# Kernel optimization log

Hardware: AMD Instinct MI355X
Metric: run time of the kernel (lower is better)

Reference implementation:

```python
import jax, jax.numpy as jnp
import numpy as np


def _derive_cayley():
    basis_gens = [(), (1,), (2,), (3,), (1, 2), (1, 3), (2, 3), (1, 2, 3)]
    gens_to_idx = {g: i for i, g in enumerate(basis_gens)}

    def reduce(a, b):
        gens = list(a) + list(b)
        sign = 1
        changed = True
        while changed:
            changed = False
            i = 0
            while i < len(gens) - 1:
                if gens[i] == gens[i + 1]:
                    gens.pop(i); gens.pop(i)
                    changed = True
                    if i > 0:
                        i -= 1
                elif gens[i] > gens[i + 1]:
                    gens[i], gens[i + 1] = gens[i + 1], gens[i]
                    sign *= -1
                    changed = True
                    i += 1
                else:
                    i += 1
        return gens_to_idx[tuple(gens)], sign

    K = np.zeros((8, 8), dtype=np.int32)   # target blade of product i*j
    S = np.zeros((8, 8), dtype=np.float32)  # sign of product i*j
    for i in range(8):
        for j in range(8):
            k, s = reduce(basis_gens[i], basis_gens[j])
            K[i, j] = k
            S[i, j] = s
    return K, S

_K, _S = _derive_cayley()
_I, _J = np.meshgrid(np.arange(8), np.arange(8), indexing='ij')
_K_FLAT = jnp.asarray(_K.reshape(-1))
_I_FLAT = jnp.asarray(_I.reshape(-1))
_J_FLAT = jnp.asarray(_J.reshape(-1))
_S_FLAT = jnp.asarray(_S.reshape(-1))

LN_EPS = 1e-5


def setup_inputs() -> dict:
    key = jax.random.key(0)
    ks = jax.random.split(key, 4)
    N_tok, D, F = 4096, 1024, 4096
    x = jax.random.normal(ks[0], (N_tok, 8, D), dtype=jnp.float32)
    interaction_weights = jnp.ones((64,), dtype=jnp.float32) * 0.1
    geo_gate = jnp.asarray(0.5, dtype=jnp.float32)
    ln_w = jnp.ones((D,), dtype=jnp.float32)
    ln_b = jnp.zeros((D,), dtype=jnp.float32)
    s = 0.02
    w_gate = jax.random.normal(ks[1], (D, F), dtype=jnp.float32) * s
    w_up = jax.random.normal(ks[2], (D, F), dtype=jnp.float32) * s
    w_down = jax.random.normal(ks[3], (F, D), dtype=jnp.float32) * s
    return {"x": x, "interaction_weights": interaction_weights, "geo_gate": geo_gate,
            "ln_w": ln_w, "ln_b": ln_b, "w_gate": w_gate, "w_up": w_up, "w_down": w_down}


def reference(x, interaction_weights, geo_gate, ln_w, ln_b, w_gate, w_up, w_down):
    dtype = x.dtype
    # sparse bilinear coefficient tensor C[k, i, j] = sign(i,j) * sigmoid(w)[i*8+j]
    w = jax.nn.sigmoid(interaction_weights).astype(dtype)  # (64,)
    C = jnp.zeros((8, 8, 8), dtype=dtype).at[_K_FLAT, _I_FLAT, _J_FLAT].set(_S_FLAT.astype(dtype) * w)
    # geometric product: geo[n,k,d] = sum_ij C[k,i,j] x[n,i,d] x[n,j,d]
    geo = jnp.einsum('kij,nid,njd->nkd', C, x, x)
    g = jax.nn.sigmoid(geo_gate).astype(dtype)
    mixed = g * geo + (1.0 - g) * x  # (N, 8, D)
    # LayerNorm over last dim D
    mu = jnp.mean(mixed, axis=-1, keepdims=True)
    var = jnp.mean(jnp.square(mixed - mu), axis=-1, keepdims=True)
    flat = (mixed - mu) * jax.lax.rsqrt(var + LN_EPS) * ln_w + ln_b
    # SwiGLU MLP
    h = jax.nn.silu(flat @ w_gate) * (flat @ w_up)  # (N, 8, F)
    out = h @ w_down  # (N, 8, D)
    return x + out
```

## Files before the change

kernel.cpp:

```cpp
#include <hip/hip_runtime.h>

typedef unsigned short u16;
using bf16x8 = __attribute__((ext_vector_type(8))) __bf16;
using f32x4  = __attribute__((ext_vector_type(4))) float;
using u16x4  = __attribute__((ext_vector_type(4))) unsigned short;

#define D_DIM 1024
#define F_DIM 4096

struct Cayley { int k[8][8]; int s[8][8]; };
constexpr Cayley make_cayley() {
    Cayley c{};
    const int gens[8][3] = {{0,0,0},{1,0,0},{2,0,0},{3,0,0},{1,2,0},{1,3,0},{2,3,0},{1,2,3}};
    const int glen[8] = {0,1,1,1,2,2,2,3};
    const int mask2idx[8] = {0,1,2,4,3,5,6,7};
    for (int i = 0; i < 8; ++i) {
        for (int j = 0; j < 8; ++j) {
            int g[6] = {0,0,0,0,0,0};
            int n = 0;
            for (int t = 0; t < glen[i]; ++t) g[n++] = gens[i][t];
            for (int t = 0; t < glen[j]; ++t) g[n++] = gens[j][t];
            int sign = 1;
            bool changed = true;
            while (changed) {
                changed = false;
                int t = 0;
                while (t + 1 < n) {
                    if (g[t] == g[t+1]) {
                        for (int u = t; u + 2 < n; ++u) g[u] = g[u+2];
                        n -= 2; changed = true;
                        if (t > 0) --t;
                    } else if (g[t] > g[t+1]) {
                        int tmp = g[t]; g[t] = g[t+1]; g[t+1] = tmp;
                        sign = -sign; changed = true; ++t;
                    } else {
                        ++t;
                    }
                }
            }
            int mask = 0;
            for (int t = 0; t < n; ++t) mask |= 1 << (g[t] - 1);
            c.k[i][j] = mask2idx[mask];
            c.s[i][j] = sign;
        }
    }
    return c;
}
constexpr Cayley CAY = make_cayley();

__device__ __forceinline__ u16 f2bf(float f) {
    unsigned u = __float_as_uint(f);
    unsigned r = 0x7FFFu + ((u >> 16) & 1u);
    return (u16)((u + r) >> 16);
}

__device__ __forceinline__ void gload16(const u16* g, const u16* l) {
    __builtin_amdgcn_global_load_lds(
        (const __attribute__((address_space(1))) void*)g,
        (__attribute__((address_space(3))) void*)l, 16, 0, 0);
}

__device__ __forceinline__ bf16x8 frag(const u16* tile, int row, int ks, int lane) {
    const int slot = ((ks << 2) + (lane >> 4)) ^ (lane & 7);
    return *(const bf16x8*)(tile + row * 64 + slot * 8);
}

__global__ __launch_bounds__(256) void transpose_kernel(
    const float* __restrict__ in, u16* __restrict__ outp, int R, int C, int mode)
{
    __shared__ float tile[32][33];
    const int tx = threadIdx.x & 31, ty = threadIdx.x >> 5;
    const int c0 = blockIdx.x * 32, r0 = blockIdx.y * 32;
    #pragma unroll
    for (int t = 0; t < 4; ++t)
        tile[ty + t*8][tx] = in[(size_t)(r0 + ty + t*8) * C + c0 + tx];
    __syncthreads();
    #pragma unroll
    for (int t = 0; t < 4; ++t) {
        const int c = c0 + ty + t*8;
        int orow;
        if (mode == 0)      orow = c;
        else if (mode == 1) orow = ((c >> 4) << 5) + (c & 15);
        else                orow = ((c >> 4) << 5) + 16 + (c & 15);
        outp[(size_t)orow * R + r0 + tx] = f2bf(tile[tx][ty + t*8]);
    }
}

__global__ __launch_bounds__(256, 2) void geo_ln_kernel(
    const float* __restrict__ x, const float* __restrict__ iw,
    const float* __restrict__ gg, const float* __restrict__ lnw,
    const float* __restrict__ lnb, u16* __restrict__ flat)
{
    __shared__ float wsig[64];
    __shared__ float red[4][16];
    const int tid = threadIdx.x;
    if (tid < 64) wsig[tid] = 1.f / (1.f + __expf(-iw[tid]));
    __syncthreads();
    const float g   = 1.f / (1.f + __expf(-gg[0]));
    const float gm1 = 1.f - g;

    float coef[64];
    #pragma unroll
    for (int t = 0; t < 64; ++t) coef[t] = (float)CAY.s[t >> 3][t & 7] * wsig[t];

    const int n  = blockIdx.x;
    const int d0 = tid * 4;
    const float* xb = x + (size_t)n * 8 * D_DIM;
    f32x4 xv[8];
    #pragma unroll
    for (int i = 0; i < 8; ++i) xv[i] = __builtin_nontemporal_load((const f32x4*)(xb + i * D_DIM + d0));

    float mix[8][4];
    #pragma unroll
    for (int s4 = 0; s4 < 4; ++s4) {
        float xs[8];
        #pragma unroll
        for (int i = 0; i < 8; ++i) xs[i] = xv[i][s4];
        float geo[8] = {0.f,0.f,0.f,0.f,0.f,0.f,0.f,0.f};
        #pragma unroll
        for (int i = 0; i < 8; ++i) {
            #pragma unroll
            for (int j = 0; j < 8; ++j) {
                geo[CAY.k[i][j]] = fmaf(coef[i*8+j] * xs[i], xs[j], geo[CAY.k[i][j]]);
            }
        }
        #pragma unroll
        for (int k = 0; k < 8; ++k) mix[k][s4] = g * geo[k] + gm1 * xs[k];
    }

    float s1[8], s2[8];
    #pragma unroll
    for (int k = 0; k < 8; ++k) {
        s1[k] = 0.f; s2[k] = 0.f;
        #pragma unroll
        for (int s4 = 0; s4 < 4; ++s4) {
            s1[k] += mix[k][s4];
            s2[k]  = fmaf(mix[k][s4], mix[k][s4], s2[k]);
        }
    }
    #pragma unroll
    for (int m = 1; m < 64; m <<= 1) {
        #pragma unroll
        for (int k = 0; k < 8; ++k) {
            s1[k] += __shfl_xor(s1[k], m, 64);
            s2[k] += __shfl_xor(s2[k], m, 64);
        }
    }
    const int wave = tid >> 6, lane = tid & 63;
    if (lane == 0) {
        #pragma unroll
        for (int k = 0; k < 8; ++k) { red[wave][k] = s1[k]; red[wave][8+k] = s2[k]; }
    }
    __syncthreads();
    float mean[8], rstd[8];
    #pragma unroll
    for (int k = 0; k < 8; ++k) {
        float a = red[0][k] + red[1][k] + red[2][k] + red[3][k];
        float b = red[0][8+k] + red[1][8+k] + red[2][8+k] + red[3][8+k];
        float mu  = a * (1.f / 1024.f);
        float var = b * (1.f / 1024.f) - mu * mu;
        mean[k] = mu;
        rstd[k] = rsqrtf(var + 1e-5f);
    }
    f32x4 lw = *(const f32x4*)(lnw + d0);
    f32x4 lb = *(const f32x4*)(lnb + d0);
    #pragma unroll
    for (int k = 0; k < 8; ++k) {
        u16x4 o;
        #pragma unroll
        for (int s4 = 0; s4 < 4; ++s4) {
            float v = (mix[k][s4] - mean[k]) * rstd[k] * lw[s4] + lb[s4];
            o[s4] = f2bf(v);
        }
        *(u16x4*)(flat + ((size_t)(n * 8 + k)) * D_DIM + d0) = o;
    }
}

template<int KDIM, bool S1, bool S2, int W1, int W4>
__device__ __forceinline__ void ktile(
    int t, const u16* __restrict__ A, const u16* __restrict__ B,
    u16 (*As)[256][64], u16 (*Bs)[256][64],
    int brow, int bcol, int wave, int lane, int wm, int wn, int fr,
    f32x4 (&acc)[8][4])
{
    const int buf = t & 1;
    const u16* At = &As[buf][0][0];
    const u16* Bt = &Bs[buf][0][0];
    const int sr = lane >> 3, sslot = (lane & 7) ^ sr;

    bf16x8 af[4][2], bf[4][2];

    #pragma unroll
    for (int m = 0; m < 4; ++m)
        #pragma unroll
        for (int ks = 0; ks < 2; ++ks)
            af[m][ks] = frag(At, wm*64 + m*16 + fr, ks, lane);
    #pragma unroll
    for (int n = 0; n < 2; ++n)
        #pragma unroll
        for (int ks = 0; ks < 2; ++ks)
            bf[n][ks] = frag(Bt, wn*32 + n*16 + fr, ks, lane);
    if (S1) {
        #pragma unroll
        for (int q = 0; q < 2; ++q) {
            const int idx_w = q*512 + wave*64;
            const int row = (idx_w >> 3) + sr;
            gload16(A + (size_t)(brow + 128 + row)*KDIM + (t+1)*64 + sslot*8,
                    &As[(t+1)&1][128][0] + idx_w*8);
        }
    }
    __builtin_amdgcn_s_setprio(1);
    #pragma unroll
    for (int m = 0; m < 4; ++m)
        #pragma unroll
        for (int n = 0; n < 2; ++n)
            #pragma unroll
            for (int ks = 0; ks < 2; ++ks)
                acc[m][n] = __builtin_amdgcn_mfma_f32_16x16x32_bf16(af[m][ks], bf[n][ks], acc[m][n], 0, 0, 0);
    __builtin_amdgcn_s_setprio(0);
    if constexpr (W1 == 6) asm volatile("s_waitcnt vmcnt(6)" ::: "memory");
    else                   asm volatile("s_waitcnt vmcnt(0)" ::: "memory");
    __builtin_amdgcn_s_barrier();
    __builtin_amdgcn_sched_barrier(0);

    #pragma unroll
    for (int n = 0; n < 2; ++n)
        #pragma unroll
        for (int ks = 0; ks < 2; ++ks)
            bf[2+n][ks] = frag(Bt, 128 + wn*32 + n*16 + fr, ks, lane);
    if (S1) {
        #pragma unroll
        for (int q = 0; q < 2; ++q) {
            const int idx_w = q*512 + wave*64;
            const int row = (idx_w >> 3) + sr;
            gload16(B + (size_t)(bcol + 128 + row)*KDIM + (t+1)*64 + sslot*8,
                    &Bs[(t+1)&1][128][0] + idx_w*8);
        }
    }
    __builtin_amdgcn_s_setprio(1);
    #pragma unroll
    for (int m = 0; m < 4; ++m)
        #pragma unroll
        for (int n = 0; n < 2; ++n)
            #pragma unroll
            for (int ks = 0; ks < 2; ++ks)
                acc[m][2+n] = __builtin_amdgcn_mfma_f32_16x16x32_bf16(af[m][ks], bf[2+n][ks], acc[m][2+n], 0, 0, 0);
    __builtin_amdgcn_s_setprio(0);
    __builtin_amdgcn_s_barrier();
    __builtin_amdgcn_sched_barrier(0);

    #pragma unroll
    for (int m = 0; m < 4; ++m)
        #pragma unroll
        for (int ks = 0; ks < 2; ++ks)
            af[m][ks] = frag(At, 128 + wm*64 + m*16 + fr, ks, lane);
    if (S2) {
        #pragma unroll
        for (int q = 0; q < 2; ++q) {
            const int idx_w = q*512 + wave*64;
            const int row = (idx_w >> 3) + sr;
            gload16(A + (size_t)(brow + row)*KDIM + (t+2)*64 + sslot*8,
                    &As[buf][0][0] + idx_w*8);
        }
    }
    __builtin_amdgcn_s_setprio(1);
    #pragma unroll
    for (int m = 0; m < 4; ++m)
        #pragma unroll
        for (int n = 0; n < 2; ++n)
            #pragma unroll
            for (int ks = 0; ks < 2; ++ks)
                acc[4+m][n] = __builtin_amdgcn_mfma_f32_16x16x32_bf16(af[m][ks], bf[n][ks], acc[4+m][n], 0, 0, 0);
    __builtin_amdgcn_s_setprio(0);
    __builtin_amdgcn_s_barrier();
    __builtin_amdgcn_sched_barrier(0);

    if (S2) {
        #pragma unroll
        for (int q = 0; q < 2; ++q) {
            const int idx_w = q*512 + wave*64;
            const int row = (idx_w >> 3) + sr;
            gload16(B + (size_t)(bcol + row)*KDIM + (t+2)*64 + sslot*8,
                    &Bs[buf][0][0] + idx_w*8);
        }
    }
    __builtin_amdgcn_s_setprio(1);
    #pragma unroll
    for (int m = 0; m < 4; ++m)
        #pragma unroll
        for (int n = 0; n < 2; ++n)
            #pragma unroll
            for (int ks = 0; ks < 2; ++ks)
                acc[4+m][2+n] = __builtin_amdgcn_mfma_f32_16x16x32_bf16(af[m][ks], bf[2+n][ks], acc[4+m][2+n], 0, 0, 0);
    __builtin_amdgcn_s_setprio(0);
    if constexpr (W4 == 8)      asm volatile("s_waitcnt vmcnt(8)" ::: "memory");
    else if constexpr (W4 == 4) asm volatile("s_waitcnt vmcnt(4)" ::: "memory");
    __builtin_amdgcn_s_barrier();
    __builtin_amdgcn_sched_barrier(0);
}

template<int KDIM, int EPI>
__global__ __launch_bounds__(512, 2) void gemm8ph(
    const u16* __restrict__ A, const u16* __restrict__ B,
    const float* __restrict__ X, void* __restrict__ OUT, int Ncols)
{
    constexpr int NT = KDIM / 64;
    __shared__ alignas(16) u16 As[2][256][64];
    __shared__ alignas(16) u16 Bs[2][256][64];

    const int nbx = Ncols >> 8;
    const int nwg = gridDim.x;
    const int bid = blockIdx.x;
    const int wg  = (bid & 7) * (nwg >> 3) + (bid >> 3);
    const int brow = (wg / nbx) << 8;
    const int bcol = (wg % nbx) << 8;

    const int tid = threadIdx.x;
    const int wave = tid >> 6, lane = tid & 63;
    const int wm = wave >> 2, wn = wave & 3;
    const int fr = lane & 15, fq = lane >> 4;
    const int sr = lane >> 3, sslot = (lane & 7) ^ sr;

    f32x4 acc[8][4];
    #pragma unroll
    for (int i = 0; i < 8; ++i)
        #pragma unroll
        for (int j = 0; j < 4; ++j) acc[i][j] = {0.f, 0.f, 0.f, 0.f};

    #pragma unroll
    for (int q = 0; q < 2; ++q) {
        const int idx_w = q*512 + wave*64;
        const int row = (idx_w >> 3) + sr;
        gload16(A + (size_t)(brow + row)*KDIM + sslot*8,          &As[0][0][0]   + idx_w*8);
    }
    #pragma unroll
    for (int q = 0; q < 2; ++q) {
        const int idx_w = q*512 + wave*64;
        const int row = (idx_w >> 3) + sr;
        gload16(B + (size_t)(bcol + row)*KDIM + sslot*8,          &Bs[0][0][0]   + idx_w*8);
    }
    #pragma unroll
    for (int q = 0; q < 2; ++q) {
        const int idx_w = q*512 + wave*64;
        const int row = (idx_w >> 3) + sr;
        gload16(A + (size_t)(brow + 128 + row)*KDIM + sslot*8,    &As[0][128][0] + idx_w*8);
    }
    #pragma unroll
    for (int q = 0; q < 2; ++q) {
        const int idx_w = q*512 + wave*64;
        const int row = (idx_w >> 3) + sr;
        gload16(B + (size_t)(bcol + 128 + row)*KDIM + sslot*8,    &Bs[0][128][0] + idx_w*8);
    }
    #pragma unroll
    for (int q = 0; q < 2; ++q) {
        const int idx_w = q*512 + wave*64;
        const int row = (idx_w >> 3) + sr;
        gload16(A + (size_t)(brow + row)*KDIM + 64 + sslot*8,     &As[1][0][0]   + idx_w*8);
    }
    #pragma unroll
    for (int q = 0; q < 2; ++q) {
        const int idx_w = q*512 + wave*64;
        const int row = (idx_w >> 3) + sr;
        gload16(B + (size_t)(bcol + row)*KDIM + 64 + sslot*8,     &Bs[1][0][0]   + idx_w*8);
    }
    asm volatile("s_waitcnt vmcnt(8)" ::: "memory");
    __builtin_amdgcn_s_barrier();
    __builtin_amdgcn_sched_barrier(0);

    #pragma unroll 1
    for (int t = 0; t < NT - 2; ++t)
        ktile<KDIM, true, true, 6, 8>(t, A, B, As, Bs, brow, bcol, wave, lane, wm, wn, fr, acc);
    ktile<KDIM, true,  false, 6, 4>(NT-2, A, B, As, Bs, brow, bcol, wave, lane, wm, wn, fr, acc);
    ktile<KDIM, false, false, 0, -1>(NT-1, A, B, As, Bs, brow, bcol, wave, lane, wm, wn, fr, acc);

    if constexpr (EPI == 1) {
        u16* H = (u16*)OUT;
        const int Nh = Ncols >> 1;
        #pragma unroll
        for (int qm = 0; qm < 2; ++qm)
            #pragma unroll
            for (int m = 0; m < 4; ++m) {
                const int row = brow + qm*128 + wm*64 + m*16 + fq*4;
                #pragma unroll
                for (int qn = 0; qn < 2; ++qn) {
                    const int col = (bcol >> 1) + qn*64 + wn*16 + fr;
                    f32x4 g = acc[qm*4+m][qn*2+0];
                    f32x4 u = acc[qm*4+m][qn*2+1];
                    #pragma unroll
                    for (int r = 0; r < 4; ++r) {
                        float gv = g[r], uv = u[r];
                        float hv = (gv / (1.f + __expf(-gv))) * uv;
                        __builtin_nontemporal_store(f2bf(hv), &H[(size_t)(row + r) * Nh + col]);
                    }
                }
            }
    } else {
        float* Of = (float*)OUT;
        #pragma unroll
        for (int mi = 0; mi < 8; ++mi) {
            const int row = brow + (mi>>2)*128 + wm*64 + (mi&3)*16 + fq*4;
            #pragma unroll
            for (int ni = 0; ni < 4; ++ni) {
                const int col = bcol + (ni>>1)*128 + wn*32 + (ni&1)*16 + fr;
                #pragma unroll
                for (int r = 0; r < 4; ++r) {
                    float xv = __builtin_nontemporal_load(&X[(size_t)(row+r)*Ncols + col]);
                    __builtin_nontemporal_store(xv + acc[mi][ni][r], &Of[(size_t)(row+r)*Ncols + col]);
                }
            }
        }
    }
}

extern "C" void kernel_launch(void* const* d_in, const int* in_sizes, int n_in,
                              void* d_out, int out_size, void* d_ws, size_t ws_size,
                              hipStream_t stream) {
    const float* x     = (const float*)d_in[0];
    const float* iw    = (const float*)d_in[1];
    const float* gg    = (const float*)d_in[2];
    const float* lnw   = (const float*)d_in[3];
    const float* lnb   = (const float*)d_in[4];
    const float* wgate = (const float*)d_in[5];
    const float* wup   = (const float*)d_in[6];
    const float* wdown = (const float*)d_in[7];
    float* out = (float*)d_out;

    const int ntok = in_sizes[0] / (8 * D_DIM);
    const int M    = ntok * 8;

    const size_t flat_b = (size_t)M * D_DIM * 2;
    const size_t wc_b   = (size_t)2 * D_DIM * F_DIM * 2;
    const size_t wd_b   = (size_t)D_DIM * F_DIM * 2;
    const size_t h_b    = (size_t)M * F_DIM * 2;
    const size_t need   = flat_b + wc_b + wd_b + h_b;
    if (ws_size < need) return;

    char* ws = (char*)d_ws;
    u16* flat = (u16*)(ws);
    u16* wc   = (u16*)(ws + flat_b);
    u16* wdt  = (u16*)(ws + flat_b + wc_b);
    u16* h    = (u16*)(ws + flat_b + wc_b + wd_b);

    transpose_kernel<<<dim3(F_DIM/32, D_DIM/32), 256, 0, stream>>>(wgate, wc,  D_DIM, F_DIM, 1);
    transpose_kernel<<<dim3(F_DIM/32, D_DIM/32), 256, 0, stream>>>(wup,   wc,  D_DIM, F_DIM, 2);
    transpose_kernel<<<dim3(D_DIM/32, F_DIM/32), 256, 0, stream>>>(wdown, wdt, F_DIM, D_DIM, 0);
    geo_ln_kernel<<<dim3(ntok), 256, 0, stream>>>(x, iw, gg, lnw, lnb, flat);

    gemm8ph<D_DIM, 1><<<dim3((M/256) * (2*F_DIM/256)), 512, 0, stream>>>(flat, wc, nullptr, h, 2*F_DIM);
    gemm8ph<F_DIM, 0><<<dim3((M/256) * (D_DIM/256)), 512, 0, stream>>>(h, wdt, x, out, D_DIM);
}
```

Baseline: 871.0 us.

## Make GEMMs persistent with 256 workgroups looping over multiple output tiles

Both GEMMs now launch 256 workgroups, and each one walks a run of output tiles: 16 row tiles for the gate/up GEMM and 2 column tiles for the down GEMM. The prefetch pipeline carries across tile boundaries and the epilogue runs inline between tiles, so the pipeline never drains and there is no per-tile launch or prologue cost. The tile-to-workgroup mapping also changes: gate/up workgroups pin a fixed column strip to each XCD, aiming to keep that weight strip cached. In exchange, the epilogue stores now sit inside the pipeline, the vmcnt wait is relaxed at tile boundaries, and load balance depends on 256 workgroups matching the number of CUs.

```diff
diff --git a/kernel.cpp b/kernel.cpp
--- a/kernel.cpp
+++ b/kernel.cpp
@@ -176,14 +176,16 @@
     }
 }
 
-template<int KDIM, bool S1, bool S2, int W1, int W4>
+template<int KDIM, bool S1, bool S2, int W1T, int W4>
 __device__ __forceinline__ void ktile(
-    int t, const u16* __restrict__ A, const u16* __restrict__ B,
+    int s, const u16* __restrict__ A, const u16* __restrict__ B,
     u16 (*As)[256][64], u16 (*Bs)[256][64],
-    int brow, int bcol, int wave, int lane, int wm, int wn, int fr,
+    int brow1, int bcol1, int k1, int brow2, int bcol2, int k2, bool bigw1,
+    int wave, int lane, int wm, int wn, int fr,
     f32x4 (&acc)[8][4])
 {
-    const int buf = t & 1;
+    const int buf = s & 1;
+    const int nbuf = (s + 1) & 1;
     const u16* At = &As[buf][0][0];
     const u16* Bt = &Bs[buf][0][0];
     const int sr = lane >> 3, sslot = (lane & 7) ^ sr;
@@ -205,8 +207,8 @@
         for (int q = 0; q < 2; ++q) {
             const int idx_w = q*512 + wave*64;
             const int row = (idx_w >> 3) + sr;
-            gload16(A + (size_t)(brow + 128 + row)*KDIM + (t+1)*64 + sslot*8,
-                    &As[(t+1)&1][128][0] + idx_w*8);
+            gload16(A + (size_t)(brow1 + 128 + row)*KDIM + k1*64 + sslot*8,
+                    &As[nbuf][128][0] + idx_w*8);
         }
     }
     __builtin_amdgcn_s_setprio(1);
@@ -218,8 +220,12 @@
             for (int ks = 0; ks < 2; ++ks)
                 acc[m][n] = __builtin_amdgcn_mfma_f32_16x16x32_bf16(af[m][ks], bf[n][ks], acc[m][n], 0, 0, 0);
     __builtin_amdgcn_s_setprio(0);
-    if constexpr (W1 == 6) asm volatile("s_waitcnt vmcnt(6)" ::: "memory");
-    else                   asm volatile("s_waitcnt vmcnt(0)" ::: "memory");
+    if constexpr (W1T == 6) {
+        if (bigw1) asm volatile("s_waitcnt vmcnt(63)" ::: "memory");
+        else       asm volatile("s_waitcnt vmcnt(6)" ::: "memory");
+    } else {
+        asm volatile("s_waitcnt vmcnt(0)" ::: "memory");
+    }
     __builtin_amdgcn_s_barrier();
     __builtin_amdgcn_sched_barrier(0);
 
@@ -233,8 +239,8 @@
         for (int q = 0; q < 2; ++q) {
             const int idx_w = q*512 + wave*64;
             const int row = (idx_w >> 3) + sr;
-            gload16(B + (size_t)(bcol + 128 + row)*KDIM + (t+1)*64 + sslot*8,
-                    &Bs[(t+1)&1][128][0] + idx_w*8);
+            gload16(B + (size_t)(bcol1 + 128 + row)*KDIM + k1*64 + sslot*8,
+                    &Bs[nbuf][128][0] + idx_w*8);
         }
     }
     __builtin_amdgcn_s_setprio(1);
@@ -259,7 +265,7 @@
         for (int q = 0; q < 2; ++q) {
             const int idx_w = q*512 + wave*64;
             const int row = (idx_w >> 3) + sr;
-            gload16(A + (size_t)(brow + row)*KDIM + (t+2)*64 + sslot*8,
+            gload16(A + (size_t)(brow2 + row)*KDIM + k2*64 + sslot*8,
                     &As[buf][0][0] + idx_w*8);
         }
     }
@@ -280,7 +286,7 @@
         for (int q = 0; q < 2; ++q) {
             const int idx_w = q*512 + wave*64;
             const int row = (idx_w >> 3) + sr;
-            gload16(B + (size_t)(bcol + row)*KDIM + (t+2)*64 + sslot*8,
+            gload16(B + (size_t)(bcol2 + row)*KDIM + k2*64 + sslot*8,
                     &Bs[buf][0][0] + idx_w*8);
         }
     }
@@ -299,80 +305,11 @@
     __builtin_amdgcn_sched_barrier(0);
 }
 
-template<int KDIM, int EPI>
-__global__ __launch_bounds__(512, 2) void gemm8ph(
-    const u16* __restrict__ A, const u16* __restrict__ B,
-    const float* __restrict__ X, void* __restrict__ OUT, int Ncols)
+template<int EPI>
+__device__ __forceinline__ void tile_epilogue(
+    f32x4 (&acc)[8][4], void* __restrict__ OUT, const float* __restrict__ X,
+    int Ncols, int browE, int bcolE, int wm, int wn, int fr, int fq)
 {
-    constexpr int NT = KDIM / 64;
-    __shared__ alignas(16) u16 As[2][256][64];
-    __shared__ alignas(16) u16 Bs[2][256][64];
-
-    const int nbx = Ncols >> 8;
-    const int nwg = gridDim.x;
-    const int bid = blockIdx.x;
-    const int wg  = (bid & 7) * (nwg >> 3) + (bid >> 3);
-    const int brow = (wg / nbx) << 8;
-    const int bcol = (wg % nbx) << 8;
-
-    const int tid = threadIdx.x;
-    const int wave = tid >> 6, lane = tid & 63;
-    const int wm = wave >> 2, wn = wave & 3;
-    const int fr = lane & 15, fq = lane >> 4;
-    const int sr = lane >> 3, sslot = (lane & 7) ^ sr;
-
-    f32x4 acc[8][4];
-    #pragma unroll
-    for (int i = 0; i < 8; ++i)
-        #pragma unroll
-        for (int j = 0; j < 4; ++j) acc[i][j] = {0.f, 0.f, 0.f, 0.f};
-
-    #pragma unroll
-    for (int q = 0; q < 2; ++q) {
-        const int idx_w = q*512 + wave*64;
-        const int row = (idx_w >> 3) + sr;
-        gload16(A + (size_t)(brow + row)*KDIM + sslot*8,          &As[0][0][0]   + idx_w*8);
-    }
-    #pragma unroll
-    for (int q = 0; q < 2; ++q) {
-        const int idx_w = q*512 + wave*64;
-        const int row = (idx_w >> 3) + sr;
-        gload16(B + (size_t)(bcol + row)*KDIM + sslot*8,          &Bs[0][0][0]   + idx_w*8);
-    }
-    #pragma unroll
-    for (int q = 0; q < 2; ++q) {
-        const int idx_w = q*512 + wave*64;
-        const int row = (idx_w >> 3) + sr;
-        gload16(A + (size_t)(brow + 128 + row)*KDIM + sslot*8,    &As[0][128][0] + idx_w*8);
-    }
-    #pragma unroll
-    for (int q = 0; q < 2; ++q) {
-        const int idx_w = q*512 + wave*64;
-        const int row = (idx_w >> 3) + sr;
-        gload16(B + (size_t)(bcol + 128 + row)*KDIM + sslot*8,    &Bs[0][128][0] + idx_w*8);
-    }
-    #pragma unroll
-    for (int q = 0; q < 2; ++q) {
-        const int idx_w = q*512 + wave*64;
-        const int row = (idx_w >> 3) + sr;
-        gload16(A + (size_t)(brow + row)*KDIM + 64 + sslot*8,     &As[1][0][0]   + idx_w*8);
-    }
-    #pragma unroll
-    for (int q = 0; q < 2; ++q) {
-        const int idx_w = q*512 + wave*64;
-        const int row = (idx_w >> 3) + sr;
-        gload16(B + (size_t)(bcol + row)*KDIM + 64 + sslot*8,     &Bs[1][0][0]   + idx_w*8);
-    }
-    asm volatile("s_waitcnt vmcnt(8)" ::: "memory");
-    __builtin_amdgcn_s_barrier();
-    __builtin_amdgcn_sched_barrier(0);
-
-    #pragma unroll 1
-    for (int t = 0; t < NT - 2; ++t)
-        ktile<KDIM, true, true, 6, 8>(t, A, B, As, Bs, brow, bcol, wave, lane, wm, wn, fr, acc);
-    ktile<KDIM, true,  false, 6, 4>(NT-2, A, B, As, Bs, brow, bcol, wave, lane, wm, wn, fr, acc);
-    ktile<KDIM, false, false, 0, -1>(NT-1, A, B, As, Bs, brow, bcol, wave, lane, wm, wn, fr, acc);
-
     if constexpr (EPI == 1) {
         u16* H = (u16*)OUT;
         const int Nh = Ncols >> 1;
@@ -380,10 +317,10 @@
         for (int qm = 0; qm < 2; ++qm)
             #pragma unroll
             for (int m = 0; m < 4; ++m) {
-                const int row = brow + qm*128 + wm*64 + m*16 + fq*4;
+                const int row = browE + qm*128 + wm*64 + m*16 + fq*4;
                 #pragma unroll
                 for (int qn = 0; qn < 2; ++qn) {
-                    const int col = (bcol >> 1) + qn*64 + wn*16 + fr;
+                    const int col = (bcolE >> 1) + qn*64 + wn*16 + fr;
                     f32x4 g = acc[qm*4+m][qn*2+0];
                     f32x4 u = acc[qm*4+m][qn*2+1];
                     #pragma unroll
@@ -398,10 +335,10 @@
         float* Of = (float*)OUT;
         #pragma unroll
         for (int mi = 0; mi < 8; ++mi) {
-            const int row = brow + (mi>>2)*128 + wm*64 + (mi&3)*16 + fq*4;
+            const int row = browE + (mi>>2)*128 + wm*64 + (mi&3)*16 + fq*4;
             #pragma unroll
             for (int ni = 0; ni < 4; ++ni) {
-                const int col = bcol + (ni>>1)*128 + wn*32 + (ni&1)*16 + fr;
+                const int col = bcolE + (ni>>1)*128 + wn*32 + (ni&1)*16 + fr;
                 #pragma unroll
                 for (int r = 0; r < 4; ++r) {
                     float xv = __builtin_nontemporal_load(&X[(size_t)(row+r)*Ncols + col]);
@@ -410,6 +347,116 @@
             }
         }
     }
+    #pragma unroll
+    for (int i = 0; i < 8; ++i)
+        #pragma unroll
+        for (int j = 0; j < 4; ++j) acc[i][j] = {0.f, 0.f, 0.f, 0.f};
+}
+
+template<int KDIM, int EPI, int TILES>
+__global__ __launch_bounds__(512, 2) void gemm8ph(
+    const u16* __restrict__ A, const u16* __restrict__ B,
+    const float* __restrict__ X, void* __restrict__ OUT, int Ncols)
+{
+    constexpr int NT  = KDIM / 64;
+    constexpr int LNT = __builtin_ctz(NT);
+    constexpr int TS  = TILES * NT;
+    __shared__ alignas(16) u16 As[2][256][64];
+    __shared__ alignas(16) u16 Bs[2][256][64];
+
+    const int bid = blockIdx.x;
+    int brow0, bcol0, drow, dcol;
+    if constexpr (EPI == 1) {
+        const int xcd = bid & 7, idx = bid >> 3;
+        brow0 = (idx >> 2) * (TILES << 8);
+        bcol0 = (xcd * 4 + (idx & 3)) << 8;
+        drow = 256; dcol = 0;
+    } else {
+        brow0 = (bid >> 1) << 8;
+        bcol0 = (bid & 1) * (TILES << 8);
+        drow = 0; dcol = 256;
+    }
+
+    const int tid = threadIdx.x;
+    const int wave = tid >> 6, lane = tid & 63;
+    const int wm = wave >> 2, wn = wave & 3;
+    const int fr = lane & 15, fq = lane >> 4;
+    const int sr = lane >> 3, sslot = (lane & 7) ^ sr;
+
+    f32x4 acc[8][4];
+    #pragma unroll
+    for (int i = 0; i < 8; ++i)
+        #pragma unroll
+        for (int j = 0; j < 4; ++j) acc[i][j] = {0.f, 0.f, 0.f, 0.f};
+
+    #pragma unroll
+    for (int q = 0; q < 2; ++q) {
+        const int idx_w = q*512 + wave*64;
+        const int row = (idx_w >> 3) + sr;
+        gload16(A + (size_t)(brow0 + row)*KDIM + sslot*8,          &As[0][0][0]   + idx_w*8);
+    }
+    #pragma unroll
+    for (int q = 0; q < 2; ++q) {
+        const int idx_w = q*512 + wave*64;
+        const int row = (idx_w >> 3) + sr;
+        gload16(B + (size_t)(bcol0 + row)*KDIM + sslot*8,          &Bs[0][0][0]   + idx_w*8);
+    }
+    #pragma unroll
+    for (int q = 0; q < 2; ++q) {
+        const int idx_w = q*512 + wave*64;
+        const int row = (idx_w >> 3) + sr;
+        gload16(A + (size_t)(brow0 + 128 + row)*KDIM + sslot*8,    &As[0][128][0] + idx_w*8);
+    }
+    #pragma unroll
+    for (int q = 0; q < 2; ++q) {
+        const int idx_w = q*512 + wave*64;
+        const int row = (idx_w >> 3) + sr;
+        gload16(B + (size_t)(bcol0 + 128 + row)*KDIM + sslot*8,    &Bs[0][128][0] + idx_w*8);
+    }
+    #pragma unroll
+    for (int q = 0; q < 2; ++q) {
+        const int idx_w = q*512 + wave*64;
+        const int row = (idx_w >> 3) + sr;
+        gload16(A + (size_t)(brow0 + row)*KDIM + 64 + sslot*8,     &As[1][0][0]   + idx_w*8);
+    }
+    #pragma unroll
+    for (int q = 0; q < 2; ++q) {
+        const int idx_w = q*512 + wave*64;
+        const int row = (idx_w >> 3) + sr;
+        gload16(B + (size_t)(bcol0 + row)*KDIM + 64 + sslot*8,     &Bs[1][0][0]   + idx_w*8);
+    }
+    asm volatile("s_waitcnt vmcnt(8)" ::: "memory");
+    __builtin_amdgcn_s_barrier();
+    __builtin_amdgcn_sched_barrier(0);
+
+    int s = 0;
+    #pragma unroll 1
+    for (; s < TS - 2; ++s) {
+        const int s1 = s + 1, s2 = s + 2;
+        const int tl1 = s1 >> LNT, k1 = s1 & (NT - 1);
+        const int tl2 = s2 >> LNT, k2 = s2 & (NT - 1);
+        const bool bigw1 = (s > 0) && ((s & (NT - 1)) == 0);
+        ktile<KDIM, true, true, 6, 8>(s, A, B, As, Bs,
+            brow0 + tl1*drow, bcol0 + tl1*dcol, k1,
+            brow0 + tl2*drow, bcol0 + tl2*dcol, k2, bigw1,
+            wave, lane, wm, wn, fr, acc);
+        if ((s1 & (NT - 1)) == 0) {
+            const int tl = s >> LNT;
+            tile_epilogue<EPI>(acc, OUT, X, Ncols, brow0 + tl*drow, bcol0 + tl*dcol, wm, wn, fr, fq);
+        }
+    }
+    {
+        const int s1 = s + 1;
+        const int tl1 = s1 >> LNT, k1 = s1 & (NT - 1);
+        ktile<KDIM, true, false, 6, 4>(s, A, B, As, Bs,
+            brow0 + tl1*drow, bcol0 + tl1*dcol, k1, 0, 0, 0, false,
+            wave, lane, wm, wn, fr, acc);
+        ++s;
+    }
+    ktile<KDIM, false, false, 0, -1>(s, A, B, As, Bs, 0, 0, 0, 0, 0, 0, false,
+        wave, lane, wm, wn, fr, acc);
+    tile_epilogue<EPI>(acc, OUT, X, Ncols,
+        brow0 + (TILES-1)*drow, bcol0 + (TILES-1)*dcol, wm, wn, fr, fq);
 }
 
 extern "C" void kernel_launch(void* const* d_in, const int* in_sizes, int n_in,
@@ -446,6 +493,6 @@
     transpose_kernel<<<dim3(D_DIM/32, F_DIM/32), 256, 0, stream>>>(wdown, wdt, F_DIM, D_DIM, 0);
     geo_ln_kernel<<<dim3(ntok), 256, 0, stream>>>(x, iw, gg, lnw, lnb, flat);
 
-    gemm8ph<D_DIM, 1><<<dim3((M/256) * (2*F_DIM/256)), 512, 0, stream>>>(flat, wc, nullptr, h, 2*F_DIM);
-    gemm8ph<F_DIM, 0><<<dim3((M/256) * (D_DIM/256)), 512, 0, stream>>>(h, wdt, x, out, D_DIM);
-}
+    gemm8ph<D_DIM, 1, 16><<<dim3(256), 512, 0, stream>>>(flat, wc, nullptr, h, 2*F_DIM);
+    gemm8ph<F_DIM, 0, 2><<<dim3(256), 512, 0, stream>>>(h, wdt, x, out, D_DIM);
+}
```

Result: slower. 957.9 us (+10.0%).

## Switch GEMM inner loop to 32x32x16 MFMA with matching weight interleave

Applied to the files above, without the earlier changes.

Replaces the 16x16x32 bf16 MFMA tiling with 32x32x16 MFMA instructions, restructuring fragment loads, accumulators (f32x16) and both epilogues to the new register layout. The gate/up weight interleave moves from 16-column to 128-column groups so each wave's accumulators hold matching gate and up columns. The fused gate/up kernel also gets a new XCD-aware block-to-tile mapping. The goal is fewer MFMA issues and fewer LDS fragment reads per FLOP, at the cost of a different LDS access pattern and a different L2 locality pattern.

```diff
diff --git a/kernel.cpp b/kernel.cpp
--- a/kernel.cpp
+++ b/kernel.cpp
@@ -3,6 +3,7 @@
 typedef unsigned short u16;
 using bf16x8 = __attribute__((ext_vector_type(8))) __bf16;
 using f32x4  = __attribute__((ext_vector_type(4))) float;
+using f32x16 = __attribute__((ext_vector_type(16))) float;
 using u16x4  = __attribute__((ext_vector_type(4))) unsigned short;
 
 #define D_DIM 1024
@@ -60,9 +61,10 @@
         (__attribute__((address_space(3))) void*)l, 16, 0, 0);
 }
 
-__device__ __forceinline__ bf16x8 frag(const u16* tile, int row, int ks, int lane) {
-    const int slot = ((ks << 2) + (lane >> 4)) ^ (lane & 7);
-    return *(const bf16x8*)(tile + row * 64 + slot * 8);
+__device__ __forceinline__ bf16x8 frag32(const u16* tile, int rowbase, int kk, int lane) {
+    const int r = rowbase + (lane & 31);
+    const int slot = ((kk << 1) + (lane >> 5)) ^ (r & 7);
+    return *(const bf16x8*)(tile + r * 64 + slot * 8);
 }
 
 __global__ __launch_bounds__(256) void transpose_kernel(
@@ -80,8 +82,8 @@
         const int c = c0 + ty + t*8;
         int orow;
         if (mode == 0)      orow = c;
-        else if (mode == 1) orow = ((c >> 4) << 5) + (c & 15);
-        else                orow = ((c >> 4) << 5) + 16 + (c & 15);
+        else if (mode == 1) orow = ((c >> 7) << 8) + (c & 127);
+        else                orow = ((c >> 7) << 8) + 128 + (c & 127);
         outp[(size_t)orow * R + r0 + tx] = f2bf(tile[tx][ty + t*8]);
     }
 }
@@ -180,26 +182,24 @@
 __device__ __forceinline__ void ktile(
     int t, const u16* __restrict__ A, const u16* __restrict__ B,
     u16 (*As)[256][64], u16 (*Bs)[256][64],
-    int brow, int bcol, int wave, int lane, int wm, int wn, int fr,
-    f32x4 (&acc)[8][4])
+    int brow, int bcol, int wave, int lane, int wm, int wn,
+    f32x16 (&acc)[4][2])
 {
     const int buf = t & 1;
     const u16* At = &As[buf][0][0];
     const u16* Bt = &Bs[buf][0][0];
     const int sr = lane >> 3, sslot = (lane & 7) ^ sr;
 
-    bf16x8 af[4][2], bf[4][2];
-
-    #pragma unroll
-    for (int m = 0; m < 4; ++m)
-        #pragma unroll
-        for (int ks = 0; ks < 2; ++ks)
-            af[m][ks] = frag(At, wm*64 + m*16 + fr, ks, lane);
-    #pragma unroll
-    for (int n = 0; n < 2; ++n)
-        #pragma unroll
-        for (int ks = 0; ks < 2; ++ks)
-            bf[n][ks] = frag(Bt, wn*32 + n*16 + fr, ks, lane);
+    bf16x8 af[2][4], bf0[4], bf1[4];
+
+    #pragma unroll
+    for (int mt = 0; mt < 2; ++mt)
+        #pragma unroll
+        for (int kk = 0; kk < 4; ++kk)
+            af[mt][kk] = frag32(At, wm*64 + mt*32, kk, lane);
+    #pragma unroll
+    for (int kk = 0; kk < 4; ++kk)
+        bf0[kk] = frag32(Bt, wn*32, kk, lane);
     if (S1) {
         #pragma unroll
         for (int q = 0; q < 2; ++q) {
@@ -211,12 +211,10 @@
     }
     __builtin_amdgcn_s_setprio(1);
     #pragma unroll
-    for (int m = 0; m < 4; ++m)
-        #pragma unroll
-        for (int n = 0; n < 2; ++n)
-            #pragma unroll
-            for (int ks = 0; ks < 2; ++ks)
-                acc[m][n] = __builtin_amdgcn_mfma_f32_16x16x32_bf16(af[m][ks], bf[n][ks], acc[m][n], 0, 0, 0);
+    for (int mt = 0; mt < 2; ++mt)
+        #pragma unroll
+        for (int kk = 0; kk < 4; ++kk)
+            acc[mt][0] = __builtin_amdgcn_mfma_f32_32x32x16_bf16(af[mt][kk], bf0[kk], acc[mt][0], 0, 0, 0);
     __builtin_amdgcn_s_setprio(0);
     if constexpr (W1 == 6) asm volatile("s_waitcnt vmcnt(6)" ::: "memory");
     else                   asm volatile("s_waitcnt vmcnt(0)" ::: "memory");
@@ -224,10 +222,8 @@
     __builtin_amdgcn_sched_barrier(0);
 
     #pragma unroll
-    for (int n = 0; n < 2; ++n)
-        #pragma unroll
-        for (int ks = 0; ks < 2; ++ks)
-            bf[2+n][ks] = frag(Bt, 128 + wn*32 + n*16 + fr, ks, lane);
+    for (int kk = 0; kk < 4; ++kk)
+        bf1[kk] = frag32(Bt, 128 + wn*32, kk, lane);
     if (S1) {
         #pragma unroll
         for (int q = 0; q < 2; ++q) {
@@ -239,21 +235,19 @@
     }
     __builtin_amdgcn_s_setprio(1);
     #pragma unroll
-    for (int m = 0; m < 4; ++m)
-        #pragma unroll
-        for (int n = 0; n < 2; ++n)
-            #pragma unroll
-            for (int ks = 0; ks < 2; ++ks)
-                acc[m][2+n] = __builtin_amdgcn_mfma_f32_16x16x32_bf16(af[m][ks], bf[2+n][ks], acc[m][2+n], 0, 0, 0);
+    for (int mt = 0; mt < 2; ++mt)
+        #pragma unroll
+        for (int kk = 0; kk < 4; ++kk)
+            acc[mt][1] = __builtin_amdgcn_mfma_f32_32x32x16_bf16(af[mt][kk], bf1[kk], acc[mt][1], 0, 0, 0);
     __builtin_amdgcn_s_setprio(0);
     __builtin_amdgcn_s_barrier();
     __builtin_amdgcn_sched_barrier(0);
 
     #pragma unroll
-    for (int m = 0; m < 4; ++m)
-        #pragma unroll
-        for (int ks = 0; ks < 2; ++ks)
-            af[m][ks] = frag(At, 128 + wm*64 + m*16 + fr, ks, lane);
+    for (int mt = 0; mt < 2; ++mt)
+        #pragma unroll
+        for (int kk = 0; kk < 4; ++kk)
+            af[mt][kk] = frag32(At, 128 + wm*64 + mt*32, kk, lane);
     if (S2) {
         #pragma unroll
         for (int q = 0; q < 2; ++q) {
@@ -265,12 +259,10 @@
     }
     __builtin_amdgcn_s_setprio(1);
     #pragma unroll
-    for (int m = 0; m < 4; ++m)
-        #pragma unroll
-        for (int n = 0; n < 2; ++n)
-            #pragma unroll
-            for (int ks = 0; ks < 2; ++ks)
-                acc[4+m][n] = __builtin_amdgcn_mfma_f32_16x16x32_bf16(af[m][ks], bf[n][ks], acc[4+m][n], 0, 0, 0);
+    for (int mt = 0; mt < 2; ++mt)
+        #pragma unroll
+        for (int kk = 0; kk < 4; ++kk)
+            acc[2+mt][0] = __builtin_amdgcn_mfma_f32_32x32x16_bf16(af[mt][kk], bf0[kk], acc[2+mt][0], 0, 0, 0);
     __builtin_amdgcn_s_setprio(0);
     __builtin_amdgcn_s_barrier();
     __builtin_amdgcn_sched_barrier(0);
@@ -286,12 +278,10 @@
     }
     __builtin_amdgcn_s_setprio(1);
     #pragma unroll
-    for (int m = 0; m < 4; ++m)
-        #pragma unroll
-        for (int n = 0; n < 2; ++n)
-            #pragma unroll
-            for (int ks = 0; ks < 2; ++ks)
-                acc[4+m][2+n] = __builtin_amdgcn_mfma_f32_16x16x32_bf16(af[m][ks], bf[2+n][ks], acc[4+m][2+n], 0, 0, 0);
+    for (int mt = 0; mt < 2; ++mt)
+        #pragma unroll
+        for (int kk = 0; kk < 4; ++kk)
+            acc[2+mt][1] = __builtin_amdgcn_mfma_f32_32x32x16_bf16(af[mt][kk], bf1[kk], acc[2+mt][1], 0, 0, 0);
     __builtin_amdgcn_s_setprio(0);
     if constexpr (W4 == 8)      asm volatile("s_waitcnt vmcnt(8)" ::: "memory");
     else if constexpr (W4 == 4) asm volatile("s_waitcnt vmcnt(4)" ::: "memory");
@@ -311,21 +301,30 @@
     const int nbx = Ncols >> 8;
     const int nwg = gridDim.x;
     const int bid = blockIdx.x;
-    const int wg  = (bid & 7) * (nwg >> 3) + (bid >> 3);
-    const int brow = (wg / nbx) << 8;
-    const int bcol = (wg % nbx) << 8;
+    int brow, bcol;
+    if constexpr (EPI == 1) {
+        const int xcd = bid & 7, idx = bid >> 3;
+        const int cpx = nbx >> 3;
+        bcol = (xcd * cpx + (idx & (cpx - 1))) << 8;
+        brow = (idx / cpx) << 8;
+    } else {
+        const int wg = (bid & 7) * (nwg >> 3) + (bid >> 3);
+        brow = (wg / nbx) << 8;
+        bcol = (wg % nbx) << 8;
+    }
 
     const int tid = threadIdx.x;
     const int wave = tid >> 6, lane = tid & 63;
     const int wm = wave >> 2, wn = wave & 3;
-    const int fr = lane & 15, fq = lane >> 4;
     const int sr = lane >> 3, sslot = (lane & 7) ^ sr;
 
-    f32x4 acc[8][4];
-    #pragma unroll
-    for (int i = 0; i < 8; ++i)
-        #pragma unroll
-        for (int j = 0; j < 4; ++j) acc[i][j] = {0.f, 0.f, 0.f, 0.f};
+    f32x16 acc[4][2];
+    #pragma unroll
+    for (int i = 0; i < 4; ++i)
+        #pragma unroll
+        for (int j = 0; j < 2; ++j)
+            #pragma unroll
+            for (int e = 0; e < 16; ++e) acc[i][j][e] = 0.f;
 
     #pragma unroll
     for (int q = 0; q < 2; ++q) {
@@ -369,46 +368,48 @@
 
     #pragma unroll 1
     for (int t = 0; t < NT - 2; ++t)
-        ktile<KDIM, true, true, 6, 8>(t, A, B, As, Bs, brow, bcol, wave, lane, wm, wn, fr, acc);
-    ktile<KDIM, true,  false, 6, 4>(NT-2, A, B, As, Bs, brow, bcol, wave, lane, wm, wn, fr, acc);
-    ktile<KDIM, false, false, 0, -1>(NT-1, A, B, As, Bs, brow, bcol, wave, lane, wm, wn, fr, acc);
-
+        ktile<KDIM, true, true, 6, 8>(t, A, B, As, Bs, brow, bcol, wave, lane, wm, wn, acc);
+    ktile<KDIM, true,  false, 6, 4>(NT-2, A, B, As, Bs, brow, bcol, wave, lane, wm, wn, acc);
+    ktile<KDIM, false, false, 0, -1>(NT-1, A, B, As, Bs, brow, bcol, wave, lane, wm, wn, acc);
+
+    const int cl = lane & 31, hi4 = (lane >> 5) * 4;
     if constexpr (EPI == 1) {
         u16* H = (u16*)OUT;
         const int Nh = Ncols >> 1;
+        const int col = (bcol >> 1) + wn*32 + cl;
         #pragma unroll
         for (int qm = 0; qm < 2; ++qm)
             #pragma unroll
-            for (int m = 0; m < 4; ++m) {
-                const int row = brow + qm*128 + wm*64 + m*16 + fq*4;
+            for (int mt = 0; mt < 2; ++mt) {
+                const int rowb = brow + qm*128 + wm*64 + mt*32 + hi4;
+                f32x16 g = acc[qm*2+mt][0];
+                f32x16 u = acc[qm*2+mt][1];
                 #pragma unroll
-                for (int qn = 0; qn < 2; ++qn) {
-                    const int col = (bcol >> 1) + qn*64 + wn*16 + fr;
-                    f32x4 g = acc[qm*4+m][qn*2+0];
-                    f32x4 u = acc[qm*4+m][qn*2+1];
-                    #pragma unroll
-                    for (int r = 0; r < 4; ++r) {
-                        float gv = g[r], uv = u[r];
-                        float hv = (gv / (1.f + __expf(-gv))) * uv;
-                        __builtin_nontemporal_store(f2bf(hv), &H[(size_t)(row + r) * Nh + col]);
-                    }
+                for (int reg = 0; reg < 16; ++reg) {
+                    const int row = rowb + (reg & 3) + 8*(reg >> 2);
+                    float gv = g[reg], uv = u[reg];
+                    float hv = (gv / (1.f + __expf(-gv))) * uv;
+                    __builtin_nontemporal_store(f2bf(hv), &H[(size_t)row * Nh + col]);
                 }
             }
     } else {
         float* Of = (float*)OUT;
         #pragma unroll
-        for (int mi = 0; mi < 8; ++mi) {
-            const int row = brow + (mi>>2)*128 + wm*64 + (mi&3)*16 + fq*4;
+        for (int qm = 0; qm < 2; ++qm)
             #pragma unroll
-            for (int ni = 0; ni < 4; ++ni) {
-                const int col = bcol + (ni>>1)*128 + wn*32 + (ni&1)*16 + fr;
+            for (int mt = 0; mt < 2; ++mt) {
+                const int rowb = brow + qm*128 + wm*64 + mt*32 + hi4;
                 #pragma unroll
-                for (int r = 0; r < 4; ++r) {
-                    float xv = __builtin_nontemporal_load(&X[(size_t)(row+r)*Ncols + col]);
-                    __builtin_nontemporal_store(xv + acc[mi][ni][r], &Of[(size_t)(row+r)*Ncols + col]);
+                for (int qn = 0; qn < 2; ++qn) {
+                    const int col = bcol + qn*128 + wn*32 + cl;
+                    #pragma unroll
+                    for (int reg = 0; reg < 16; ++reg) {
+                        const int row = rowb + (reg & 3) + 8*(reg >> 2);
+                        float xv = __builtin_nontemporal_load(&X[(size_t)row*Ncols + col]);
+                        __builtin_nontemporal_store(xv + acc[qm*2+mt][qn][reg], &Of[(size_t)row*Ncols + col]);
+                    }
                 }
             }
-        }
     }
 }
 
```

After: 941.6 us. 8.1% more time.

## Restructure GEMM k-tile into two phases and remap gate/up tiles per XCD

Applied to the files above, without the earlier changes.

Merges the four-phase k-tile schedule into two phases. Each phase loads both B fragment halves up front and issues 32 MFMAs per barrier instead of 16, with the waitcnt thresholds adjusted to match. This halves the barriers per k-tile but holds more B fragments in registers, which could hurt occupancy at 2 waves/SIMD. For the gate/up GEMM, it also remaps workgroups so each XCD owns a contiguous band of columns, aiming for better L2 reuse of weights.

```diff
diff --git a/kernel.cpp b/kernel.cpp
--- a/kernel.cpp
+++ b/kernel.cpp
@@ -176,19 +176,20 @@
     }
 }
 
-template<int KDIM, bool S1, bool S2, int W1, int W4>
-__device__ __forceinline__ void ktile(
+template<int KDIM, bool S1, bool S2, int W>
+__device__ __forceinline__ void ktile2(
     int t, const u16* __restrict__ A, const u16* __restrict__ B,
     u16 (*As)[256][64], u16 (*Bs)[256][64],
     int brow, int bcol, int wave, int lane, int wm, int wn, int fr,
     f32x4 (&acc)[8][4])
 {
     const int buf = t & 1;
+    const int nbuf = (t + 1) & 1;
     const u16* At = &As[buf][0][0];
     const u16* Bt = &Bs[buf][0][0];
     const int sr = lane >> 3, sslot = (lane & 7) ^ sr;
 
-    bf16x8 af[4][2], bf[4][2];
+    bf16x8 af[4][2], bf0[2][2], bf1[2][2];
 
     #pragma unroll
     for (int m = 0; m < 4; ++m)
@@ -198,43 +199,24 @@
     #pragma unroll
     for (int n = 0; n < 2; ++n)
         #pragma unroll
-        for (int ks = 0; ks < 2; ++ks)
-            bf[n][ks] = frag(Bt, wn*32 + n*16 + fr, ks, lane);
+        for (int ks = 0; ks < 2; ++ks) {
+            bf0[n][ks] = frag(Bt, wn*32 + n*16 + fr, ks, lane);
+            bf1[n][ks] = frag(Bt, 128 + wn*32 + n*16 + fr, ks, lane);
+        }
     if (S1) {
         #pragma unroll
         for (int q = 0; q < 2; ++q) {
             const int idx_w = q*512 + wave*64;
             const int row = (idx_w >> 3) + sr;
             gload16(A + (size_t)(brow + 128 + row)*KDIM + (t+1)*64 + sslot*8,
-                    &As[(t+1)&1][128][0] + idx_w*8);
-        }
-    }
-    __builtin_amdgcn_s_setprio(1);
-    #pragma unroll
-    for (int m = 0; m < 4; ++m)
-        #pragma unroll
-        for (int n = 0; n < 2; ++n)
-            #pragma unroll
-            for (int ks = 0; ks < 2; ++ks)
-                acc[m][n] = __builtin_amdgcn_mfma_f32_16x16x32_bf16(af[m][ks], bf[n][ks], acc[m][n], 0, 0, 0);
-    __builtin_amdgcn_s_setprio(0);
-    if constexpr (W1 == 6) asm volatile("s_waitcnt vmcnt(6)" ::: "memory");
-    else                   asm volatile("s_waitcnt vmcnt(0)" ::: "memory");
-    __builtin_amdgcn_s_barrier();
-    __builtin_amdgcn_sched_barrier(0);
-
-    #pragma unroll
-    for (int n = 0; n < 2; ++n)
-        #pragma unroll
-        for (int ks = 0; ks < 2; ++ks)
-            bf[2+n][ks] = frag(Bt, 128 + wn*32 + n*16 + fr, ks, lane);
-    if (S1) {
+                    &As[nbuf][128][0] + idx_w*8);
+        }
         #pragma unroll
         for (int q = 0; q < 2; ++q) {
             const int idx_w = q*512 + wave*64;
             const int row = (idx_w >> 3) + sr;
             gload16(B + (size_t)(bcol + 128 + row)*KDIM + (t+1)*64 + sslot*8,
-                    &Bs[(t+1)&1][128][0] + idx_w*8);
+                    &Bs[nbuf][128][0] + idx_w*8);
         }
     }
     __builtin_amdgcn_s_setprio(1);
@@ -243,8 +225,10 @@
         #pragma unroll
         for (int n = 0; n < 2; ++n)
             #pragma unroll
-            for (int ks = 0; ks < 2; ++ks)
-                acc[m][2+n] = __builtin_amdgcn_mfma_f32_16x16x32_bf16(af[m][ks], bf[2+n][ks], acc[m][2+n], 0, 0, 0);
+            for (int ks = 0; ks < 2; ++ks) {
+                acc[m][n]   = __builtin_amdgcn_mfma_f32_16x16x32_bf16(af[m][ks], bf0[n][ks], acc[m][n],   0, 0, 0);
+                acc[m][2+n] = __builtin_amdgcn_mfma_f32_16x16x32_bf16(af[m][ks], bf1[n][ks], acc[m][2+n], 0, 0, 0);
+            }
     __builtin_amdgcn_s_setprio(0);
     __builtin_amdgcn_s_barrier();
     __builtin_amdgcn_sched_barrier(0);
@@ -262,20 +246,6 @@
             gload16(A + (size_t)(brow + row)*KDIM + (t+2)*64 + sslot*8,
                     &As[buf][0][0] + idx_w*8);
         }
-    }
-    __builtin_amdgcn_s_setprio(1);
-    #pragma unroll
-    for (int m = 0; m < 4; ++m)
-        #pragma unroll
-        for (int n = 0; n < 2; ++n)
-            #pragma unroll
-            for (int ks = 0; ks < 2; ++ks)
-                acc[4+m][n] = __builtin_amdgcn_mfma_f32_16x16x32_bf16(af[m][ks], bf[n][ks], acc[4+m][n], 0, 0, 0);
-    __builtin_amdgcn_s_setprio(0);
-    __builtin_amdgcn_s_barrier();
-    __builtin_amdgcn_sched_barrier(0);
-
-    if (S2) {
         #pragma unroll
         for (int q = 0; q < 2; ++q) {
             const int idx_w = q*512 + wave*64;
@@ -290,11 +260,13 @@
         #pragma unroll
         for (int n = 0; n < 2; ++n)
             #pragma unroll
-            for (int ks = 0; ks < 2; ++ks)
-                acc[4+m][2+n] = __builtin_amdgcn_mfma_f32_16x16x32_bf16(af[m][ks], bf[2+n][ks], acc[4+m][2+n], 0, 0, 0);
+            for (int ks = 0; ks < 2; ++ks) {
+                acc[4+m][n]   = __builtin_amdgcn_mfma_f32_16x16x32_bf16(af[m][ks], bf0[n][ks], acc[4+m][n],   0, 0, 0);
+                acc[4+m][2+n] = __builtin_amdgcn_mfma_f32_16x16x32_bf16(af[m][ks], bf1[n][ks], acc[4+m][2+n], 0, 0, 0);
+            }
     __builtin_amdgcn_s_setprio(0);
-    if constexpr (W4 == 8)      asm volatile("s_waitcnt vmcnt(8)" ::: "memory");
-    else if constexpr (W4 == 4) asm volatile("s_waitcnt vmcnt(4)" ::: "memory");
+    if constexpr (W == 4)      asm volatile("s_waitcnt vmcnt(4)" ::: "memory");
+    else if constexpr (W == 0) asm volatile("s_waitcnt vmcnt(0)" ::: "memory");
     __builtin_amdgcn_s_barrier();
     __builtin_amdgcn_sched_barrier(0);
 }
@@ -311,9 +283,17 @@
     const int nbx = Ncols >> 8;
     const int nwg = gridDim.x;
     const int bid = blockIdx.x;
-    const int wg  = (bid & 7) * (nwg >> 3) + (bid >> 3);
-    const int brow = (wg / nbx) << 8;
-    const int bcol = (wg % nbx) << 8;
+    int brow, bcol;
+    if constexpr (EPI == 1) {
+        const int xcd = bid & 7, idx = bid >> 3;
+        const int cpx = nbx >> 3;
+        bcol = (xcd * cpx + (idx & (cpx - 1))) << 8;
+        brow = (idx / cpx) << 8;
+    } else {
+        const int wg = (bid & 7) * (nwg >> 3) + (bid >> 3);
+        brow = (wg / nbx) << 8;
+        bcol = (wg % nbx) << 8;
+    }
 
     const int tid = threadIdx.x;
     const int wave = tid >> 6, lane = tid & 63;
@@ -363,15 +343,15 @@
         const int row = (idx_w >> 3) + sr;
         gload16(B + (size_t)(bcol + row)*KDIM + 64 + sslot*8,     &Bs[1][0][0]   + idx_w*8);
     }
-    asm volatile("s_waitcnt vmcnt(8)" ::: "memory");
+    asm volatile("s_waitcnt vmcnt(4)" ::: "memory");
     __builtin_amdgcn_s_barrier();
     __builtin_amdgcn_sched_barrier(0);
 
     #pragma unroll 1
     for (int t = 0; t < NT - 2; ++t)
-        ktile<KDIM, true, true, 6, 8>(t, A, B, As, Bs, brow, bcol, wave, lane, wm, wn, fr, acc);
-    ktile<KDIM, true,  false, 6, 4>(NT-2, A, B, As, Bs, brow, bcol, wave, lane, wm, wn, fr, acc);
-    ktile<KDIM, false, false, 0, -1>(NT-1, A, B, As, Bs, brow, bcol, wave, lane, wm, wn, fr, acc);
+        ktile2<KDIM, true, true, 4>(t, A, B, As, Bs, brow, bcol, wave, lane, wm, wn, fr, acc);
+    ktile2<KDIM, true,  false, 0>(NT-2, A, B, As, Bs, brow, bcol, wave, lane, wm, wn, fr, acc);
+    ktile2<KDIM, false, false, -1>(NT-1, A, B, As, Bs, brow, bcol, wave, lane, wm, wn, fr, acc);
 
     if constexpr (EPI == 1) {
         u16* H = (u16*)OUT;
```

Result: faster. 832.2 us (-4.5%).
